# Performance work log

Hardware: AMD Instinct MI355X
Metric: run time of the kernel (lower is better)

Reference implementation:

```python
import jax, jax.numpy as jnp
import numpy as np

DIM = 2048
NUM_HEADS = 16
NUM_KV_HEADS = 4
HEAD_DIM = DIM // NUM_HEADS  # 128
GROUP = NUM_HEADS // NUM_KV_HEADS  # queries per kv head
B, N = 2, 2048


def setup_inputs() -> dict:
    key = jax.random.key(0)
    ks = jax.random.split(key, 5)
    s = 1.0 / np.sqrt(DIM)
    return {
        "x": jax.random.normal(ks[0], (B, N, DIM), dtype=jnp.float32),
        "Wq": jax.random.normal(ks[1], (DIM, DIM), dtype=jnp.float32) * s,
        "Wk": jax.random.normal(ks[2], (DIM, NUM_KV_HEADS * HEAD_DIM), dtype=jnp.float32) * s,
        "Wv": jax.random.normal(ks[3], (DIM, NUM_KV_HEADS * HEAD_DIM), dtype=jnp.float32) * s,
        "Wo": jax.random.normal(ks[4], (DIM, DIM), dtype=jnp.float32) * s,
    }


def reference(x, Wq, Wk, Wv, Wo):
    Bc, Nc, C = x.shape
    scale = HEAD_DIM ** -0.5
    # projections -> [B, H, N, D] / [B, Hkv, N, D]
    q = (x @ Wq).reshape(Bc, Nc, NUM_HEADS, HEAD_DIM).transpose(0, 2, 1, 3)
    k = (x @ Wk).reshape(Bc, Nc, NUM_KV_HEADS, HEAD_DIM).transpose(0, 2, 1, 3)
    v = (x @ Wv).reshape(Bc, Nc, NUM_KV_HEADS, HEAD_DIM).transpose(0, 2, 1, 3)
    # repeat_interleave over head dim: kv head i serves query heads [i*G, (i+1)*G)
    k = jnp.repeat(k, GROUP, axis=1)  # [B, H, N, D]
    v = jnp.repeat(v, GROUP, axis=1)
    attn = jnp.einsum("bhqd,bhkd->bhqk", q, k) * scale
    attn = jax.nn.softmax(attn, axis=-1)
    out = jnp.einsum("bhqk,bhkd->bhqd", attn, v)  # [B, H, N, D]
    out = out.transpose(0, 2, 1, 3).reshape(Bc, Nc, C)
    return out @ Wo
```

## Files before the change

kernel.cpp:

```cpp
#include <hip/hip_runtime.h>
#include <hip/hip_bf16.h>
#include <cstdint>
#include <cstddef>

typedef __bf16 bf16;
typedef __attribute__((ext_vector_type(8))) __bf16 bf16x8;
typedef __attribute__((ext_vector_type(4))) float f32x4;
typedef __attribute__((ext_vector_type(16))) float f32x16;
typedef unsigned int u32;
typedef __attribute__((ext_vector_type(2))) unsigned int u32x2;

#define DEVINL __device__ __forceinline__

DEVINL void gload16(const void* g, void* l) {
  __builtin_amdgcn_global_load_lds(
      (const __attribute__((address_space(1))) void*)g,
      (__attribute__((address_space(3))) void*)l, 16, 0, 0);
}

DEVINL f32x4 mfma16(bf16x8 a, bf16x8 b, f32x4 c) {
  return __builtin_amdgcn_mfma_f32_16x16x32_bf16(a, b, c, 0, 0, 0);
}
DEVINL f32x16 mfma32(bf16x8 a, bf16x8 b, f32x16 c) {
  return __builtin_amdgcn_mfma_f32_32x32x16_bf16(a, b, c, 0, 0, 0);
}
DEVINL u32 cvtpk(float lo, float hi) {
  u32 r;
  asm("v_cvt_pk_bf16_f32 %0, %1, %2" : "=v"(r) : "v"(lo), "v"(hi));
  return r;
}
DEVINL void plswap(u32& a, u32& b) {
  asm("v_permlane32_swap_b32 %0, %1" : "+v"(a), "+v"(b));
}

__global__ __launch_bounds__(256) void prep_kernel(const float* __restrict__ x,
                                                   const float* __restrict__ Wq,
                                                   const float* __restrict__ Wk,
                                                   const float* __restrict__ Wv,
                                                   const float* __restrict__ Wo,
                                                   bf16* __restrict__ xbf,
                                                   bf16* __restrict__ WqkvT,
                                                   bf16* __restrict__ WoT) {
  const int bid = blockIdx.x, t = threadIdx.x;
  if (bid < 4096) {
    int i = bid * 256 + t;
    f32x4 a = ((const f32x4*)x)[2 * i];
    f32x4 b2 = ((const f32x4*)x)[2 * i + 1];
    bf16x8 v;
#pragma unroll
    for (int k = 0; k < 4; ++k) { v[k] = (bf16)a[k]; v[4 + k] = (bf16)b2[k]; }
    ((bf16x8*)xbf)[i] = v;
    return;
  }
  __shared__ float tile[64][65];
  const float* src;
  bf16* dst;
  int N, blk;
  if (bid < 5120)      { src = Wq; dst = WqkvT;                        N = 2048; blk = bid - 4096; }
  else if (bid < 5376) { src = Wk; dst = WqkvT + (size_t)2048 * 2048;  N = 512;  blk = bid - 5120; }
  else if (bid < 5632) { src = Wv; dst = WqkvT + (size_t)2560 * 2048;  N = 512;  blk = bid - 5376; }
  else                 { src = Wo; dst = WoT;                          N = 2048; blk = bid - 5632; }
  const int K = 2048;
  int nt = N >> 6;
  int n0 = (blk % nt) << 6;
  int k0 = (blk / nt) << 6;
  int c = t & 63, rb = t >> 6;
#pragma unroll
  for (int rr = 0; rr < 16; ++rr) {
    int row = rr * 4 + rb;
    tile[row][c] = src[(size_t)(k0 + row) * N + n0 + c];
  }
  __syncthreads();
#pragma unroll
  for (int rr = 0; rr < 16; ++rr) {
    int nrow = rr * 4 + rb;
    dst[(size_t)(n0 + nrow) * K + k0 + c] = (bf16)tile[c][nrow];
  }
}

template <int EPI>
__global__ __launch_bounds__(256) void gemm_bt_kernel(const bf16* __restrict__ A,
                                                      const bf16* __restrict__ BT,
                                                      float* __restrict__ Cout,
                                                      int Mtiles,
                                                      bf16* __restrict__ qb,
                                                      bf16* __restrict__ kb_,
                                                      bf16* __restrict__ vtb) {
  __shared__ __align__(16) unsigned char smem[49152];
  const int t = threadIdx.x, w = t >> 6, lane = t & 63;
  const int l4 = lane >> 4, l16 = lane & 15;
  const int swz = (blockIdx.x & 7) * ((int)gridDim.x >> 3) + (blockIdx.x >> 3);
  const int bm = swz % Mtiles, bn = swz / Mtiles;
  const int wm = w >> 1, wn = w & 1;

  const char* aP[2];
  const char* bP[2];
#pragma unroll
  for (int p = 0; p < 2; ++p) {
    int g = p * 256 + t;
    aP[p] = (const char*)A + (size_t)(bm * 128 + (g >> 2)) * 4096 + (g & 3) * 16;
    bP[p] = (const char*)BT + (size_t)(bn * 128 + (g >> 2)) * 4096 + (g & 3) * 16;
  }
  const unsigned ldsW = w * 1024;

  auto STAGE = [&](unsigned off, int k0) {
    gload16(aP[0] + k0, smem + off + ldsW);
    gload16(aP[1] + k0, smem + off + 4096 + ldsW);
    gload16(bP[0] + k0, smem + off + 8192 + ldsW);
    gload16(bP[1] + k0, smem + off + 12288 + ldsW);
  };

  const f32x4 fz = {0.f, 0.f, 0.f, 0.f};
  f32x4 acc[4][4];
#pragma unroll
  for (int i = 0; i < 4; ++i)
#pragma unroll
    for (int j = 0; j < 4; ++j) acc[i][j] = fz;

  const int arow = 64 * wm + l16, brow = 64 * wn + l16, kbyte = 16 * l4;

  STAGE(0, 0);
  STAGE(16384, 64);
  asm volatile("s_waitcnt vmcnt(4)" ::: "memory");
  __builtin_amdgcn_s_barrier();
  __builtin_amdgcn_sched_barrier(0);

  unsigned off0 = 0, off1 = 16384, off2 = 32768;
#pragma unroll 1
  for (int tt = 0; tt < 64; ++tt) {
    if (tt < 62) STAGE(off2, (tt + 2) * 64);
    bf16x8 af[4], bfr[4];
#pragma unroll
    for (int i = 0; i < 4; ++i)
      af[i] = *(const bf16x8*)(smem + off0 + (arow + 16 * i) * 64 + kbyte);
#pragma unroll
    for (int j = 0; j < 4; ++j)
      bfr[j] = *(const bf16x8*)(smem + off0 + 8192 + (brow + 16 * j) * 64 + kbyte);
#pragma unroll
    for (int i = 0; i < 4; ++i)
#pragma unroll
      for (int j = 0; j < 4; ++j)
        acc[i][j] = mfma16(af[i], bfr[j], acc[i][j]);
    if (tt < 63) {
      if (tt < 62) asm volatile("s_waitcnt vmcnt(4)" ::: "memory");
      else         asm volatile("s_waitcnt vmcnt(0)" ::: "memory");
      __builtin_amdgcn_s_barrier();
      __builtin_amdgcn_sched_barrier(0);
    }
    unsigned tmp = off0; off0 = off1; off1 = off2; off2 = tmp;
  }

  const int r0 = bm * 128 + 64 * wm + 4 * l4;
  if (EPI == 1) {
#pragma unroll
    for (int j = 0; j < 4; ++j) {
      int col = bn * 128 + 64 * wn + 16 * j + l16;
#pragma unroll
      for (int i = 0; i < 4; ++i)
#pragma unroll
        for (int r = 0; r < 4; ++r)
          Cout[(size_t)(r0 + 16 * i + r) * 2048 + col] = acc[i][j][r];
    }
  } else {
    const int bq = bm >> 4;
#pragma unroll
    for (int j = 0; j < 4; ++j) {
      int col = bn * 128 + 64 * wn + 16 * j + l16;
      if (bn < 16) {
        int hh = col >> 7, d = col & 127;
        bf16* dst = qb + (size_t)((bq * 16 + hh) * 2048) * 128 + d;
#pragma unroll
        for (int i = 0; i < 4; ++i)
#pragma unroll
          for (int r = 0; r < 4; ++r) {
            int n = (r0 + 16 * i + r) & 2047;
            dst[(size_t)n * 128] = (bf16)acc[i][j][r];
          }
      } else if (bn < 20) {
        int kv = (col >> 7) - 16, d = col & 127;
        bf16* dst = kb_ + (size_t)((bq * 4 + kv) * 2048) * 128 + d;
#pragma unroll
        for (int i = 0; i < 4; ++i)
#pragma unroll
          for (int r = 0; r < 4; ++r) {
            int n = (r0 + 16 * i + r) & 2047;
            dst[(size_t)n * 128] = (bf16)acc[i][j][r];
          }
      } else {
        int kv = (col >> 7) - 20, d = col & 127;
        bf16* dst = vtb + ((size_t)(bq * 4 + kv) * 128 + d) * 2048;
#pragma unroll
        for (int i = 0; i < 4; ++i)
#pragma unroll
          for (int r = 0; r < 4; ++r) {
            int n = (r0 + 16 * i + r) & 2047;
            dst[n] = (bf16)acc[i][j][r];
          }
      }
    }
  }
}

__global__ __launch_bounds__(256, 2) void attn_kernel(const bf16* __restrict__ Q,
                                                      const bf16* __restrict__ K,
                                                      const bf16* __restrict__ VT,
                                                      bf16* __restrict__ AO) {
  __shared__ __align__(16) unsigned char smem[65536];
  const int t = threadIdx.x, w = t >> 6, lane = t & 63;
  const int q = lane & 31, hi = lane >> 5;
  const int pair = blockIdx.x >> 4;
  const int q00 = (blockIdx.x & 15) * 128 + w * 32;
  const int b = pair >> 4, h = pair & 15, kvh = h >> 2;
  const float KS2 = 0.08838834764831845f * 1.4426950408889634f;

  bf16x8 qf[8];
  {
    const char* qbase = (const char*)Q +
        ((size_t)((b * 16 + h) * 2048 + q00 + q) * 128 + 8 * hi) * 2;
#pragma unroll
    for (int dk = 0; dk < 8; ++dk) qf[dk] = *(const bf16x8*)(qbase + dk * 32);
  }

  f32x16 acc[4];
#pragma unroll
  for (int dt = 0; dt < 4; ++dt)
#pragma unroll
    for (int r = 0; r < 16; ++r) acc[dt][r] = 0.0f;
  float mrun = -1e30f, lrun = 0.0f;

  const char* Kg = (const char*)K + (size_t)((b * 4 + kvh) * 2048) * 256;
  const char* Vg = (const char*)VT + (size_t)((b * 4 + kvh) * 128) * 4096;

  auto STAGE_K = [&](int itn) {
    const unsigned base = (unsigned)(itn & 1) * 16384u;
    const int kb = itn * 64;
#pragma unroll
    for (int p = 0; p < 4; ++p) {
      int g = p * 256 + t;
      int row = g >> 4, cb = (g & 15) * 16;
      gload16(Kg + (size_t)(kb + row) * 256 + (cb ^ ((row & 15) << 4)),
              smem + base + p * 4096 + w * 1024);
    }
  };
  auto STAGE_V = [&](int itn) {
    const unsigned base = 32768u + (unsigned)(itn & 1) * 16384u;
    const int kb = itn * 64;
#pragma unroll
    for (int p = 0; p < 4; ++p) {
      int g = p * 256 + t;
      int row = g >> 3, cb = (g & 7) * 16;
      gload16(Vg + (size_t)row * 4096 + kb * 2 + (cb ^ ((row & 7) << 4)),
              smem + base + p * 4096 + w * 1024);
    }
  };

  auto SMFMA = [&](int itn, f32x16& s0, f32x16& s1) {
    const unsigned base = (unsigned)(itn & 1) * 16384u;
    const unsigned swq = (q & 15) << 4;
#pragma unroll
    for (int r = 0; r < 16; ++r) { s0[r] = 0.0f; s1[r] = 0.0f; }
    __builtin_amdgcn_s_setprio(1);
#pragma unroll
    for (int dk = 0; dk < 8; ++dk) {
      const int cb = dk * 32 + 16 * hi;
      bf16x8 k0 = *(const bf16x8*)(smem + base + q * 256 + (cb ^ swq));
      bf16x8 k1 = *(const bf16x8*)(smem + base + (q + 32) * 256 + (cb ^ swq));
      s0 = mfma32(k0, qf[dk], s0);
      s1 = mfma32(k1, qf[dk], s1);
    }
    __builtin_amdgcn_s_setprio(0);
  };

  auto FINISH = [&](int itn, f32x16& s0, f32x16& s1) {
    float tm[16];
#pragma unroll
    for (int r = 0; r < 16; ++r) tm[r] = fmaxf(s0[r], s1[r]);
#pragma unroll
    for (int st = 8; st; st >>= 1)
#pragma unroll
      for (int r = 0; r < 8; ++r)
        if (r < st) tm[r] = fmaxf(tm[r], tm[r + st]);
    float mo = tm[0];
    mo = fmaxf(mo, __shfl_xor(mo, 32, 64));
    if (!__all((mo - mrun) * KS2 <= 8.0f)) {
      float mn = fmaxf(mrun, mo);
      float al = __builtin_amdgcn_exp2f((mrun - mn) * KS2);
      lrun *= al;
#pragma unroll
      for (int dt = 0; dt < 4; ++dt)
#pragma unroll
        for (int r = 0; r < 16; ++r) acc[dt][r] *= al;
      mrun = mn;
    }
    const float c0 = KS2 * mrun;
    float p0[16], p1[16];
#pragma unroll
    for (int r = 0; r < 16; ++r) {
      p0[r] = __builtin_amdgcn_exp2f(s0[r] * KS2 - c0);
      p1[r] = __builtin_amdgcn_exp2f(s1[r] * KS2 - c0);
    }
    float ts[16];
#pragma unroll
    for (int r = 0; r < 16; ++r) ts[r] = p0[r] + p1[r];
#pragma unroll
    for (int st = 8; st; st >>= 1)
#pragma unroll
      for (int r = 0; r < 8; ++r)
        if (r < st) ts[r] += ts[r + st];
    float rs = ts[0];
    rs += __shfl_xor(rs, 32, 64);
    lrun += rs;

    bf16x8 pa[4];
#pragma unroll
    for (int ks = 0; ks < 4; ++ks) {
      const int bs = (ks & 1) * 8;
      float* P = (ks >> 1) ? p1 : p0;
      u32 A0 = cvtpk(P[bs + 0], P[bs + 1]);
      u32 A1 = cvtpk(P[bs + 2], P[bs + 3]);
      u32 B0 = cvtpk(P[bs + 4], P[bs + 5]);
      u32 B1 = cvtpk(P[bs + 6], P[bs + 7]);
      plswap(A0, B0);
      plswap(A1, B1);
      union { u32 u[4]; bf16x8 v; } pu;
      pu.u[0] = A0; pu.u[1] = A1; pu.u[2] = B0; pu.u[3] = B1;
      pa[ks] = pu.v;
    }

    const unsigned vbase = 32768u + (unsigned)(itn & 1) * 16384u;
    __builtin_amdgcn_s_setprio(1);
#pragma unroll
    for (int ks = 0; ks < 4; ++ks) {
      const int kcol = ks * 32 + 16 * hi;
      const unsigned swd = (q & 7) << 4;
      bf16x8 va0 = *(const bf16x8*)(smem + vbase + (0 * 32 + q) * 128 + (kcol ^ swd));
      bf16x8 va1 = *(const bf16x8*)(smem + vbase + (1 * 32 + q) * 128 + (kcol ^ swd));
      bf16x8 va2 = *(const bf16x8*)(smem + vbase + (2 * 32 + q) * 128 + (kcol ^ swd));
      bf16x8 va3 = *(const bf16x8*)(smem + vbase + (3 * 32 + q) * 128 + (kcol ^ swd));
      acc[0] = mfma32(va0, pa[ks], acc[0]);
      acc[1] = mfma32(va1, pa[ks], acc[1]);
      acc[2] = mfma32(va2, pa[ks], acc[2]);
      acc[3] = mfma32(va3, pa[ks], acc[3]);
    }
    __builtin_amdgcn_s_setprio(0);
  };

  f32x16 sA0, sA1, sB0, sB1;
  STAGE_K(0);
  __syncthreads();

  STAGE_K(1);
  STAGE_V(0);
  SMFMA(0, sA0, sA1);
  __syncthreads();

#pragma unroll 1
  for (int i = 1; i < 31; i += 2) {
    STAGE_K(i + 1);
    STAGE_V(i);
    SMFMA(i, sB0, sB1);
    FINISH(i - 1, sA0, sA1);
    __syncthreads();
    STAGE_K(i + 2);
    STAGE_V(i + 1);
    SMFMA(i + 1, sA0, sA1);
    FINISH(i, sB0, sB1);
    __syncthreads();
  }

  STAGE_V(31);
  SMFMA(31, sB0, sB1);
  FINISH(30, sA0, sA1);
  __syncthreads();
  FINISH(31, sB0, sB1);

  const float inv = 1.0f / lrun;
  bf16* aorow = AO + (size_t)(b * 2048 + q00 + q) * 2048 + h * 128;
#pragma unroll
  for (int dt = 0; dt < 4; ++dt)
#pragma unroll
    for (int rq = 0; rq < 4; ++rq) {
      u32 w0 = cvtpk(acc[dt][rq * 4 + 0] * inv, acc[dt][rq * 4 + 1] * inv);
      u32 w1 = cvtpk(acc[dt][rq * 4 + 2] * inv, acc[dt][rq * 4 + 3] * inv);
      u32x2 pr; pr.x = w0; pr.y = w1;
      *(u32x2*)(aorow + dt * 32 + rq * 8 + 4 * hi) = pr;
    }
}

extern "C" void kernel_launch(void* const* d_in, const int* in_sizes, int n_in,
                              void* d_out, int out_size, void* d_ws, size_t ws_size,
                              hipStream_t stream) {
  const float* x = (const float*)d_in[0];
  const float* Wq = (const float*)d_in[1];
  const float* Wk = (const float*)d_in[2];
  const float* Wv = (const float*)d_in[3];
  const float* Wo = (const float*)d_in[4];

  char* ws = (char*)d_ws;
  bf16* xbf = (bf16*)(ws);
  bf16* WqkvT = (bf16*)(ws + 16777216);
  bf16* WoT = (bf16*)(ws + 29360128);
  bf16* Qbuf = (bf16*)(ws + 37748736);
  bf16* Kbuf = (bf16*)(ws + 54525952);
  bf16* VTbuf = (bf16*)(ws + 58720256);

  prep_kernel<<<6656, 256, 0, stream>>>(x, Wq, Wk, Wv, Wo, xbf, WqkvT, WoT);
  gemm_bt_kernel<0><<<768, 256, 0, stream>>>(xbf, WqkvT, nullptr, 32, Qbuf, Kbuf, VTbuf);
  attn_kernel<<<512, 256, 0, stream>>>(Qbuf, Kbuf, VTbuf, xbf);
  gemm_bt_kernel<1><<<512, 256, 0, stream>>>(xbf, WoT, (float*)d_out, 32, nullptr, nullptr, nullptr);
}
```

Measured before the change: 213.2 us.

## Interleave QK and PV MFMAs in attention; simplify GEMM to double buffering

```diff
diff --git a/kernel.cpp b/kernel.cpp
--- a/kernel.cpp
+++ b/kernel.cpp
@@ -86,11 +86,10 @@
                                                       bf16* __restrict__ qb,
                                                       bf16* __restrict__ kb_,
                                                       bf16* __restrict__ vtb) {
-  __shared__ __align__(16) unsigned char smem[49152];
+  __shared__ __align__(16) unsigned char smem[32768];
   const int t = threadIdx.x, w = t >> 6, lane = t & 63;
   const int l4 = lane >> 4, l16 = lane & 15;
-  const int swz = (blockIdx.x & 7) * ((int)gridDim.x >> 3) + (blockIdx.x >> 3);
-  const int bm = swz % Mtiles, bn = swz / Mtiles;
+  const int bm = blockIdx.x % Mtiles, bn = blockIdx.x / Mtiles;
   const int wm = w >> 1, wn = w & 1;
 
   const char* aP[2];
@@ -103,11 +102,11 @@
   }
   const unsigned ldsW = w * 1024;
 
-  auto STAGE = [&](unsigned off, int k0) {
-    gload16(aP[0] + k0, smem + off + ldsW);
-    gload16(aP[1] + k0, smem + off + 4096 + ldsW);
-    gload16(bP[0] + k0, smem + off + 8192 + ldsW);
-    gload16(bP[1] + k0, smem + off + 12288 + ldsW);
+  auto STAGE = [&](unsigned buf, int k0) {
+    gload16(aP[0] + k0, smem + buf * 16384 + ldsW);
+    gload16(aP[1] + k0, smem + buf * 16384 + 4096 + ldsW);
+    gload16(bP[0] + k0, smem + buf * 16384 + 8192 + ldsW);
+    gload16(bP[1] + k0, smem + buf * 16384 + 12288 + ldsW);
   };
 
   const f32x4 fz = {0.f, 0.f, 0.f, 0.f};
@@ -120,34 +119,25 @@
   const int arow = 64 * wm + l16, brow = 64 * wn + l16, kbyte = 16 * l4;
 
   STAGE(0, 0);
-  STAGE(16384, 64);
-  asm volatile("s_waitcnt vmcnt(4)" ::: "memory");
-  __builtin_amdgcn_s_barrier();
-  __builtin_amdgcn_sched_barrier(0);
-
-  unsigned off0 = 0, off1 = 16384, off2 = 32768;
-#pragma unroll 1
+  __syncthreads();
+
+#pragma unroll 2
   for (int tt = 0; tt < 64; ++tt) {
-    if (tt < 62) STAGE(off2, (tt + 2) * 64);
+    const unsigned buf = tt & 1;
+    if (tt < 63) STAGE(buf ^ 1u, (tt + 1) * 64);
     bf16x8 af[4], bfr[4];
 #pragma unroll
     for (int i = 0; i < 4; ++i)
-      af[i] = *(const bf16x8*)(smem + off0 + (arow + 16 * i) * 64 + kbyte);
+      af[i] = *(const bf16x8*)(smem + buf * 16384 + (arow + 16 * i) * 64 + kbyte);
 #pragma unroll
     for (int j = 0; j < 4; ++j)
-      bfr[j] = *(const bf16x8*)(smem + off0 + 8192 + (brow + 16 * j) * 64 + kbyte);
+      bfr[j] = *(const bf16x8*)(smem + buf * 16384 + 8192 + (brow + 16 * j) * 64 + kbyte);
 #pragma unroll
     for (int i = 0; i < 4; ++i)
 #pragma unroll
       for (int j = 0; j < 4; ++j)
         acc[i][j] = mfma16(af[i], bfr[j], acc[i][j]);
-    if (tt < 63) {
-      if (tt < 62) asm volatile("s_waitcnt vmcnt(4)" ::: "memory");
-      else         asm volatile("s_waitcnt vmcnt(0)" ::: "memory");
-      __builtin_amdgcn_s_barrier();
-      __builtin_amdgcn_sched_barrier(0);
-    }
-    unsigned tmp = off0; off0 = off1; off1 = off2; off2 = tmp;
+    __syncthreads();
   }
 
   const int r0 = bm * 128 + 64 * wm + 4 * l4;
@@ -271,7 +261,7 @@
     __builtin_amdgcn_s_setprio(0);
   };
 
-  auto FINISH = [&](int itn, f32x16& s0, f32x16& s1) {
+  auto SOFTMAX = [&](f32x16& s0, f32x16& s1, bf16x8* pa) {
     float tm[16];
 #pragma unroll
     for (int r = 0; r < 16; ++r) tm[r] = fmaxf(s0[r], s1[r]);
@@ -310,8 +300,6 @@
     float rs = ts[0];
     rs += __shfl_xor(rs, 32, 64);
     lrun += rs;
-
-    bf16x8 pa[4];
 #pragma unroll
     for (int ks = 0; ks < 4; ++ks) {
       const int bs = (ks & 1) * 8;
@@ -326,13 +314,44 @@
       pu.u[0] = A0; pu.u[1] = A1; pu.u[2] = B0; pu.u[3] = B1;
       pa[ks] = pu.v;
     }
-
+  };
+
+  auto FUSED = [&](int itn, f32x16& sP0, f32x16& sP1, f32x16& sN0, f32x16& sN1) {
+    bf16x8 pa[4];
+    SOFTMAX(sP0, sP1, pa);
+    const unsigned kbase = (unsigned)(itn & 1) * 16384u;
+    const unsigned vbase = 32768u + (unsigned)((itn - 1) & 1) * 16384u;
+    const unsigned swq = (q & 15) << 4;
+    const unsigned swd = (q & 7) << 4;
+#pragma unroll
+    for (int r = 0; r < 16; ++r) { sN0[r] = 0.0f; sN1[r] = 0.0f; }
+    __builtin_amdgcn_s_setprio(1);
+#pragma unroll
+    for (int step = 0; step < 8; ++step) {
+      const int cb = step * 32 + 16 * hi;
+      bf16x8 k0 = *(const bf16x8*)(smem + kbase + q * 256 + (cb ^ swq));
+      bf16x8 k1 = *(const bf16x8*)(smem + kbase + (q + 32) * 256 + (cb ^ swq));
+      const int ks = step >> 1, dt0 = (step & 1) * 2, dt1 = dt0 + 1;
+      const int kcol = ks * 32 + 16 * hi;
+      bf16x8 va0 = *(const bf16x8*)(smem + vbase + (dt0 * 32 + q) * 128 + (kcol ^ swd));
+      bf16x8 va1 = *(const bf16x8*)(smem + vbase + (dt1 * 32 + q) * 128 + (kcol ^ swd));
+      sN0 = mfma32(k0, qf[step], sN0);
+      acc[dt0] = mfma32(va0, pa[ks], acc[dt0]);
+      sN1 = mfma32(k1, qf[step], sN1);
+      acc[dt1] = mfma32(va1, pa[ks], acc[dt1]);
+    }
+    __builtin_amdgcn_s_setprio(0);
+  };
+
+  auto FINLAST = [&](int itn, f32x16& sP0, f32x16& sP1) {
+    bf16x8 pa[4];
+    SOFTMAX(sP0, sP1, pa);
     const unsigned vbase = 32768u + (unsigned)(itn & 1) * 16384u;
+    const unsigned swd = (q & 7) << 4;
     __builtin_amdgcn_s_setprio(1);
 #pragma unroll
     for (int ks = 0; ks < 4; ++ks) {
       const int kcol = ks * 32 + 16 * hi;
-      const unsigned swd = (q & 7) << 4;
       bf16x8 va0 = *(const bf16x8*)(smem + vbase + (0 * 32 + q) * 128 + (kcol ^ swd));
       bf16x8 va1 = *(const bf16x8*)(smem + vbase + (1 * 32 + q) * 128 + (kcol ^ swd));
       bf16x8 va2 = *(const bf16x8*)(smem + vbase + (2 * 32 + q) * 128 + (kcol ^ swd));
@@ -358,21 +377,18 @@
   for (int i = 1; i < 31; i += 2) {
     STAGE_K(i + 1);
     STAGE_V(i);
-    SMFMA(i, sB0, sB1);
-    FINISH(i - 1, sA0, sA1);
+    FUSED(i, sA0, sA1, sB0, sB1);
     __syncthreads();
     STAGE_K(i + 2);
     STAGE_V(i + 1);
-    SMFMA(i + 1, sA0, sA1);
-    FINISH(i, sB0, sB1);
+    FUSED(i + 1, sB0, sB1, sA0, sA1);
     __syncthreads();
   }
 
   STAGE_V(31);
-  SMFMA(31, sB0, sB1);
-  FINISH(30, sA0, sA1);
+  FUSED(31, sA0, sA1, sB0, sB1);
   __syncthreads();
-  FINISH(31, sB0, sB1);
+  FINLAST(31, sB0, sB1);
 
   const float inv = 1.0f / lrun;
   bf16* aorow = AO + (size_t)(b * 2048 + q00 + q) * 2048 + h * 128;
```

New measurement: 203.2 us. 4.7% less time.
